# Kernel optimization log

Measured on AMD Instinct MI355X. Metric: run time of the kernel, lower is better.

## Reference

```python
import jax, jax.numpy as jnp
import numpy as np

NUM_EXPERTS = 64
TOP_K = 2
NOISE_STD = 1.0
LOAD_BALANCE_WEIGHT = 0.01
NOISE_KEY = jax.random.fold_in(jax.random.key(0), 12345)


def setup_inputs() -> dict:
    key = jax.random.key(0)
    k1, k2, k3 = jax.random.split(key, 3)
    B, S, D = 4, 4096, 1024
    x = jax.random.normal(k1, (B, S, D), dtype=jnp.float32)
    W_gate = jax.random.normal(k2, (NUM_EXPERTS, D), dtype=jnp.float32) * (1.0 / np.sqrt(D))
    W_noise = jax.random.normal(k3, (NUM_EXPERTS, D), dtype=jnp.float32) * (1.0 / np.sqrt(D))
    return {"x": x, "W_gate": W_gate, "W_noise": W_noise}


def reference(x, W_gate, W_noise):
    # x: [B,S,D], W_gate/W_noise: [E,D] (torch Linear weight layout)
    clean_logits = jnp.einsum("bsd,ed->bse", x, W_gate)           # [B,S,E]
    noise_scale = jax.nn.softplus(jnp.einsum("bsd,ed->bse", x, W_noise))
    noise = jax.random.normal(NOISE_KEY, clean_logits.shape, clean_logits.dtype)
    logits = clean_logits + noise * noise_scale * NOISE_STD

    probs = jax.nn.softmax(logits, axis=-1)                        # [B,S,E]
    routing_weights, expert_indices = jax.lax.top_k(probs, TOP_K)  # [B,S,K]
    routing_weights = routing_weights / jnp.sum(routing_weights, axis=-1, keepdims=True)

    # Load-balance loss on clean logits
    B, S, E = clean_logits.shape
    num_tokens = B * S
    expert_mask = jax.nn.one_hot(expert_indices, E, dtype=jnp.float32).sum(axis=2)  # [B,S,E]
    tokens_per_expert = expert_mask.sum(axis=(0, 1))               # [E]
    fraction_tokens = tokens_per_expert / num_tokens
    router_probs = jax.nn.softmax(clean_logits, axis=-1)
    mean_router_prob = router_probs.mean(axis=(0, 1))              # [E]
    load_balance_loss = LOAD_BALANCE_WEIGHT * E * jnp.sum(fraction_tokens * mean_router_prob)

    noise_scale_mean = noise_scale.mean()
    return (routing_weights, expert_indices, load_balance_loss, router_probs, noise_scale_mean)
```

## Files before the change

kernel.cpp:

```cpp
#include <hip/hip_runtime.h>
#include <stdint.h>

#define TOKENS 16384
#define DDIM   1024
#define NEXP   64
#define NCOL   128
#define TB     32
#define NBLK   (TOKENS / TB)
#define NCH    (DDIM / 32)
#define NTILE  8
#define CPP    8

typedef __attribute__((ext_vector_type(8))) short bf16x8;
typedef __attribute__((ext_vector_type(4))) float f32x4;

__device__ ushort g_wf[3][NTILE][NCH][64][8];
__device__ float g_ps[NEXP];
__device__ float g_cnt[NEXP];
__device__ float g_spa[1];

__device__ inline ushort bf16rne(float f) {
  uint32_t u = __float_as_uint(f);
  return (ushort)((u + 0x7fffu + ((u >> 16) & 1u)) >> 16);
}
__device__ inline float bf16tof(ushort h) {
  return __uint_as_float(((uint32_t)h) << 16);
}
__device__ inline void split3(float v, ushort& h, ushort& m, ushort& l) {
  h = bf16rne(v);
  float r1 = v - bf16tof(h);
  m = bf16rne(r1);
  float r2 = r1 - bf16tof(m);
  l = bf16rne(r2);
}

struct U2 { uint32_t a, b; };

__host__ __device__ constexpr U2 tf2x32(uint32_t k0, uint32_t k1,
                                        uint32_t x0, uint32_t x1) {
  uint32_t ks[3] = {k0, k1, k0 ^ k1 ^ 0x1BD11BDAu};
  const uint32_t rot[2][4] = {{13u, 15u, 26u, 6u}, {17u, 29u, 16u, 24u}};
  x0 += ks[0]; x1 += ks[1];
  for (int d = 0; d < 5; ++d) {
    for (int j = 0; j < 4; ++j) {
      uint32_t r = rot[d & 1][j];
      x0 += x1;
      x1 = (x1 << r) | (x1 >> (32u - r));
      x1 ^= x0;
    }
    x0 += ks[(d + 1) % 3];
    x1 += ks[(d + 2) % 3] + (uint32_t)(d + 1);
  }
  return U2{x0, x1};
}

__device__ inline uint32_t noise_bits(uint32_t i) {
  constexpr U2 NK = tf2x32(0u, 0u, 0u, 12345u);
  U2 o = tf2x32(NK.a, NK.b, 0u, i);
  return o.a ^ o.b;
}

__device__ inline float xla_erfinv(float x) {
  float w = -log1pf(-x * x);
  float p;
  if (w < 5.0f) {
    w = w - 2.5f;
    p = 2.81022636e-08f;
    p = 3.43273939e-07f + p * w;
    p = -3.5233877e-06f + p * w;
    p = -4.39150654e-06f + p * w;
    p = 0.00021858087f + p * w;
    p = -0.00125372503f + p * w;
    p = -0.00417768164f + p * w;
    p = 0.246640727f + p * w;
    p = 1.50140941f + p * w;
  } else {
    w = sqrtf(w) - 3.0f;
    p = -0.000200214257f;
    p = 0.000100950558f + p * w;
    p = 0.00134934322f + p * w;
    p = -0.00367342844f + p * w;
    p = 0.00573950773f + p * w;
    p = -0.0076224613f + p * w;
    p = 0.00943887047f + p * w;
    p = 1.00167406f + p * w;
    p = 2.83297682f + p * w;
  }
  return p * x;
}

__device__ inline float noise_normal(uint32_t i) {
  uint32_t bits = noise_bits(i);
  float f = __uint_as_float((bits >> 9) | 0x3f800000u) - 1.0f;
  float u = f * 2.0f + (-0.99999994f);
  u = fmaxf(u, -0.99999994f);
  return 1.41421356237f * xla_erfinv(u);
}

__device__ inline float softplus_ref(float x) {
  return fmaxf(x, 0.0f) + log1pf(expf(-fabsf(x)));
}

__device__ inline float wave_max64(float v) {
  #pragma unroll
  for (int off = 32; off; off >>= 1) v = fmaxf(v, __shfl_xor(v, off, 64));
  return v;
}
__device__ inline float wave_sum64(float v) {
  #pragma unroll
  for (int off = 32; off; off >>= 1) v += __shfl_xor(v, off, 64);
  return v;
}
__device__ inline void wave_argmax64(float v, int idx, float& mv, int& mi) {
  float bv = v; int bi = idx;
  #pragma unroll
  for (int off = 32; off; off >>= 1) {
    float ov = __shfl_xor(bv, off, 64);
    int   oi = __shfl_xor(bi, off, 64);
    if (ov > bv || (ov == bv && oi < bi)) { bv = ov; bi = oi; }
  }
  mv = bv; mi = bi;
}

__global__ __launch_bounds__(64)
void wsplit_kernel(const float* __restrict__ wg, const float* __restrict__ wn) {
  const int ct   = blockIdx.x >> 5;
  const int kc   = blockIdx.x & 31;
  const int lane = threadIdx.x;
  const int col  = ct * 16 + (lane & 15);
  const int koff = kc * 32 + (lane >> 4) * 8;
  const float* src = (col < NEXP) ? (wg + (size_t)col * DDIM)
                                  : (wn + (size_t)(col - NEXP) * DDIM);
  const float4 v0 = *(const float4*)&src[koff];
  const float4 v1 = *(const float4*)&src[koff + 4];
  const float av[8] = {v0.x, v0.y, v0.z, v0.w, v1.x, v1.y, v1.z, v1.w};
  union BF8 { bf16x8 v; ushort u[8]; };
  BF8 H, M, L;
  #pragma unroll
  for (int j = 0; j < 8; ++j) {
    ushort h, m, l;
    split3(av[j], h, m, l);
    H.u[j] = h; M.u[j] = m; L.u[j] = l;
  }
  *(bf16x8*)&g_wf[0][ct][kc][lane][0] = H.v;
  *(bf16x8*)&g_wf[1][ct][kc][lane][0] = M.v;
  *(bf16x8*)&g_wf[2][ct][kc][lane][0] = L.v;

  if (blockIdx.x == 0) {
    g_ps[lane] = 0.0f; g_cnt[lane] = 0.0f;
    if (lane == 0) g_spa[0] = 0.0f;
  }
}

__global__ __launch_bounds__(1024, 8)
void NoisyTopKRouter_57621281243491_kernel(
    const float* __restrict__ x, float* __restrict__ out) {
  __shared__ ushort ldsA[3][2][CPP][64][8];

  const int tid  = threadIdx.x;
  const int w    = tid >> 6;
  const int lane = tid & 63;
  const int tg   = w & 1;
  const int ct   = w >> 1;
  const int tok0 = blockIdx.x * TB;

  char* LA = (char*)&ldsA[0][0][0][0][0];

  const int srow = tid >> 5;
  const int skq  = tid & 31;
  const int stg  = srow >> 4;
  const int sfr  = srow & 15;
  const int sc   = skq >> 2;
  const int ss   = skq & 3;
  const int so   = (sc * 1024 + ss * 256 + sfr * 16) ^ ((skq & 15) << 4);
  const float* sx = x + (size_t)(tok0 + srow) * DDIM + skq * 8;

  const int fr_row = lane & 15;
  const int fr_s   = lane >> 4;
  const ushort* wf = &g_wf[0][0][0][0][0];
  const int b0 = ct * 16384 + lane * 8;
  #define PS 131072
  const int abase = tg * 8192;

  f32x4 acc = {0.f, 0.f, 0.f, 0.f};

  float4 xa0, xa1, xb0, xb1;

  #define SPLIT_PHASE(X0, X1)                                             \
    {                                                                     \
      union BF8 { bf16x8 v; ushort u[8]; };                               \
      BF8 H, M, L;                                                        \
      const float av_[8] = {X0.x, X0.y, X0.z, X0.w, X1.x, X1.y, X1.z, X1.w}; \
      _Pragma("unroll")                                                   \
      for (int j = 0; j < 8; ++j) {                                       \
        ushort h_, m_, l_;                                                \
        split3(av_[j], h_, m_, l_);                                       \
        H.u[j] = h_; M.u[j] = m_; L.u[j] = l_;                            \
      }                                                                   \
      *(bf16x8*)(LA + stg * 8192 + so)         = H.v;                     \
      *(bf16x8*)(LA + 16384 + stg * 8192 + so) = M.v;                     \
      *(bf16x8*)(LA + 32768 + stg * 8192 + so) = L.v;                     \
    }

  #define MFMA_PHASE(ph)                                                  \
    _Pragma("unroll")                                                     \
    for (int c = 0; c < CPP; ++c) {                                       \
      int ro = c * 1024 + lane * 16;                                      \
      ro ^= ((ro >> 8) & 15) << 4;                                        \
      const bf16x8 Ah = *(const bf16x8*)(LA + abase + ro);                \
      const bf16x8 Am = *(const bf16x8*)(LA + 16384 + abase + ro);        \
      const bf16x8 Al = *(const bf16x8*)(LA + 32768 + abase + ro);        \
      const int co = ((ph) * CPP + c) * 512;                              \
      const bf16x8 Bh = *(const bf16x8*)&wf[b0 + co];                     \
      const bf16x8 Bm = *(const bf16x8*)&wf[b0 + PS + co];                \
      const bf16x8 Bl = *(const bf16x8*)&wf[b0 + 2 * PS + co];            \
      acc = __builtin_amdgcn_mfma_f32_16x16x32_bf16(Ah, Bh, acc, 0, 0, 0); \
      acc = __builtin_amdgcn_mfma_f32_16x16x32_bf16(Ah, Bm, acc, 0, 0, 0); \
      acc = __builtin_amdgcn_mfma_f32_16x16x32_bf16(Am, Bh, acc, 0, 0, 0); \
      acc = __builtin_amdgcn_mfma_f32_16x16x32_bf16(Ah, Bl, acc, 0, 0, 0); \
      acc = __builtin_amdgcn_mfma_f32_16x16x32_bf16(Al, Bh, acc, 0, 0, 0); \
      acc = __builtin_amdgcn_mfma_f32_16x16x32_bf16(Am, Bm, acc, 0, 0, 0); \
    }

  #define DO_PHASE(ph, C0, C1, N0, N1, PRE)                               \
    SPLIT_PHASE(C0, C1);                                                  \
    if (PRE) {                                                            \
      N0 = *(const float4*)&sx[(ph + 1) * 256];                           \
      N1 = *(const float4*)&sx[(ph + 1) * 256 + 4];                       \
    }                                                                     \
    __syncthreads();                                                      \
    MFMA_PHASE(ph);                                                       \
    __syncthreads();

  xa0 = *(const float4*)&sx[0];
  xa1 = *(const float4*)&sx[4];

  DO_PHASE(0, xa0, xa1, xb0, xb1, 1);
  DO_PHASE(1, xb0, xb1, xa0, xa1, 1);
  DO_PHASE(2, xa0, xa1, xb0, xb1, 1);
  DO_PHASE(3, xb0, xb1, xa0, xa1, 0);

  #undef DO_PHASE
  #undef SPLIT_PHASE
  #undef MFMA_PHASE
  #undef PS

  float (*lds_logits)[NCOL + 4] = (float (*)[NCOL + 4])LA;
  float (*lps)[NEXP] = (float (*)[NEXP])(LA + 16896);
  float (*lcb)[NEXP] = (float (*)[NEXP])(LA + 20992);
  float* lspw        = (float*)(LA + 25088);

  #pragma unroll
  for (int r = 0; r < 4; ++r)
    lds_logits[tg * 16 + 4 * fr_s + r][ct * 16 + fr_row] = acc[r];
  __syncthreads();

  float* out_rw  = out;
  float* out_idx = out + 2 * TOKENS;
  float* out_rp  = out + 4 * TOKENS + 1;

  float ps_acc = 0.0f, sp_acc = 0.0f, c_acc = 0.0f;

  for (int it = 0; it < 2; ++it) {
    const int tl = w * 2 + it;
    const int t  = tok0 + tl;
    const float cl = lds_logits[tl][lane];
    const float nl = lds_logits[tl][NEXP + lane];

    const float m  = wave_max64(cl);
    const float v  = expf(cl - m);
    const float Z  = wave_sum64(v);
    const float rp = v / Z;
    out_rp[(size_t)t * NEXP + lane] = rp;
    ps_acc += rp;

    const float ns  = softplus_ref(nl);
    sp_acc += ns;
    const float noi = noise_normal((uint32_t)(t * NEXP + lane));
    const float lgn = __fadd_rn(cl, __fmul_rn(noi, ns));

    const float m2 = wave_max64(lgn);
    const float v2 = expf(lgn - m2);
    const float Z2 = wave_sum64(v2);
    const float p  = v2 / Z2;

    float p1; int i1;
    wave_argmax64(p, lane, p1, i1);
    const float pm = (lane == i1) ? -3.402823466e38f : p;
    float p2; int i2;
    wave_argmax64(pm, lane, p2, i2);

    c_acc += (float)((lane == i1) + (lane == i2));

    if (lane == 0) {
      const float s = p1 + p2;
      out_rw[t * 2 + 0]  = p1 / s;
      out_rw[t * 2 + 1]  = p2 / s;
      out_idx[t * 2 + 0] = (float)i1;
      out_idx[t * 2 + 1] = (float)i2;
    }
  }

  lps[w][lane] = ps_acc;
  lcb[w][lane] = c_acc;
  const float spw = wave_sum64(sp_acc);
  if (lane == 0) lspw[w] = spw;
  __syncthreads();
  if (tid < NEXP) {
    float a = 0.0f, b = 0.0f;
    #pragma unroll
    for (int j = 0; j < 16; ++j) { a += lps[j][tid]; b += lcb[j][tid]; }
    atomicAdd(&g_ps[tid],  a);
    atomicAdd(&g_cnt[tid], b);
  }
  if (tid == 0) {
    float s = 0.0f;
    #pragma unroll
    for (int j = 0; j < 16; ++j) s += lspw[j];
    atomicAdd(&g_spa[0], s);
  }
}

__global__ void finalize_kernel(float* __restrict__ out) {
  const int lane = threadIdx.x;
  float term = (g_cnt[lane] / (float)TOKENS) * (g_ps[lane] / (float)TOKENS);
  #pragma unroll
  for (int off = 32; off; off >>= 1) term += __shfl_xor(term, off, 64);
  if (lane == 0) {
    out[4 * TOKENS] = 0.64f * term;
    out[4 * TOKENS + 1 + TOKENS * NEXP] = g_spa[0] / (float)(TOKENS * NEXP);
  }
}

extern "C" void kernel_launch(void* const* d_in, const int* in_sizes, int n_in,
                              void* d_out, int out_size, void* d_ws, size_t ws_size,
                              hipStream_t stream) {
  const float* x  = (const float*)d_in[0];
  const float* wg = (const float*)d_in[1];
  const float* wn = (const float*)d_in[2];
  float* out = (float*)d_out;

  (void)d_ws; (void)ws_size; (void)in_sizes; (void)n_in; (void)out_size;

  wsplit_kernel<<<NTILE * NCH, 64, 0, stream>>>(wg, wn);
  NoisyTopKRouter_57621281243491_kernel<<<NBLK, 1024, 0, stream>>>(x, out);
  finalize_kernel<<<1, 64, 0, stream>>>(out);
}
```

Before: 144.7 us.

## Fuse weight split and finalize into main kernel using global atomic flags

Removes the separate weight-split and finalize launches. The first 256 blocks of the main kernel now split the weights into bf16 hi/mid/lo parts and signal a global counter, and every block spin-waits on that counter before computing. The last block to finish, found with an atomic ticket, computes the load-balance loss and the noise-scale mean and resets the counters. This saves two kernel launches and their gaps, but every block now depends on the weight-producing blocks being scheduled, since the grid of 512 blocks of 1024 threads must not deadlock. All blocks also pay for the spin-wait and the extra syncs.

```diff
diff --git a/kernel.cpp b/kernel.cpp
--- a/kernel.cpp
+++ b/kernel.cpp
@@ -18,6 +18,8 @@
 __device__ float g_ps[NEXP];
 __device__ float g_cnt[NEXP];
 __device__ float g_spa[1];
+__device__ unsigned g_wdone;
+__device__ unsigned g_done;
 
 __device__ inline ushort bf16rne(float f) {
   uint32_t u = __float_as_uint(f);
@@ -122,49 +124,64 @@
   mv = bv; mi = bi;
 }
 
-__global__ __launch_bounds__(64)
-void wsplit_kernel(const float* __restrict__ wg, const float* __restrict__ wn) {
-  const int ct   = blockIdx.x >> 5;
-  const int kc   = blockIdx.x & 31;
-  const int lane = threadIdx.x;
-  const int col  = ct * 16 + (lane & 15);
-  const int koff = kc * 32 + (lane >> 4) * 8;
-  const float* src = (col < NEXP) ? (wg + (size_t)col * DDIM)
-                                  : (wn + (size_t)(col - NEXP) * DDIM);
-  const float4 v0 = *(const float4*)&src[koff];
-  const float4 v1 = *(const float4*)&src[koff + 4];
-  const float av[8] = {v0.x, v0.y, v0.z, v0.w, v1.x, v1.y, v1.z, v1.w};
-  union BF8 { bf16x8 v; ushort u[8]; };
-  BF8 H, M, L;
-  #pragma unroll
-  for (int j = 0; j < 8; ++j) {
-    ushort h, m, l;
-    split3(av[j], h, m, l);
-    H.u[j] = h; M.u[j] = m; L.u[j] = l;
-  }
-  *(bf16x8*)&g_wf[0][ct][kc][lane][0] = H.v;
-  *(bf16x8*)&g_wf[1][ct][kc][lane][0] = M.v;
-  *(bf16x8*)&g_wf[2][ct][kc][lane][0] = L.v;
-
-  if (blockIdx.x == 0) {
-    g_ps[lane] = 0.0f; g_cnt[lane] = 0.0f;
-    if (lane == 0) g_spa[0] = 0.0f;
-  }
-}
-
 __global__ __launch_bounds__(1024, 8)
 void NoisyTopKRouter_57621281243491_kernel(
-    const float* __restrict__ x, float* __restrict__ out) {
+    const float* __restrict__ x, const float* __restrict__ wg,
+    const float* __restrict__ wn, float* __restrict__ out) {
   __shared__ ushort ldsA[3][2][CPP][64][8];
 
   const int tid  = threadIdx.x;
+  const int bid  = blockIdx.x;
   const int w    = tid >> 6;
   const int lane = tid & 63;
   const int tg   = w & 1;
   const int ct   = w >> 1;
-  const int tok0 = blockIdx.x * TB;
+  const int tok0 = bid * TB;
 
   char* LA = (char*)&ldsA[0][0][0][0][0];
+
+  if (bid < NTILE * NCH) {
+    if (tid < 64) {
+      const int act  = bid >> 5;
+      const int akc  = bid & 31;
+      const int col  = act * 16 + (tid & 15);
+      const int koff = akc * 32 + (tid >> 4) * 8;
+      const float* src = (col < NEXP) ? (wg + (size_t)col * DDIM)
+                                      : (wn + (size_t)(col - NEXP) * DDIM);
+      const float4 v0 = *(const float4*)&src[koff];
+      const float4 v1 = *(const float4*)&src[koff + 4];
+      const float av[8] = {v0.x, v0.y, v0.z, v0.w, v1.x, v1.y, v1.z, v1.w};
+      union BF8 { bf16x8 v; ushort u[8]; };
+      BF8 H, M, L;
+      #pragma unroll
+      for (int j = 0; j < 8; ++j) {
+        ushort h, m, l;
+        split3(av[j], h, m, l);
+        H.u[j] = h; M.u[j] = m; L.u[j] = l;
+      }
+      *(bf16x8*)&g_wf[0][act][akc][tid][0] = H.v;
+      *(bf16x8*)&g_wf[1][act][akc][tid][0] = M.v;
+      *(bf16x8*)&g_wf[2][act][akc][tid][0] = L.v;
+    }
+    if (bid == 0) {
+      if (tid >= 64 && tid < 128) { g_ps[tid - 64] = 0.0f; g_cnt[tid - 64] = 0.0f; }
+      if (tid == 128) g_spa[0] = 0.0f;
+    }
+    __syncthreads();
+    if (tid == 0) {
+      __threadfence();
+      __hip_atomic_fetch_add(&g_wdone, 1u, __ATOMIC_RELEASE,
+                             __HIP_MEMORY_SCOPE_AGENT);
+    }
+  }
+
+  if (tid == 0) {
+    while (__hip_atomic_load(&g_wdone, __ATOMIC_ACQUIRE,
+                             __HIP_MEMORY_SCOPE_AGENT) < (unsigned)(NTILE * NCH))
+      __builtin_amdgcn_s_sleep(2);
+    __threadfence();
+  }
+  __syncthreads();
 
   const int srow = tid >> 5;
   const int skq  = tid & 31;
@@ -319,16 +336,34 @@
     for (int j = 0; j < 16; ++j) s += lspw[j];
     atomicAdd(&g_spa[0], s);
   }
-}
-
-__global__ void finalize_kernel(float* __restrict__ out) {
-  const int lane = threadIdx.x;
-  float term = (g_cnt[lane] / (float)TOKENS) * (g_ps[lane] / (float)TOKENS);
-  #pragma unroll
-  for (int off = 32; off; off >>= 1) term += __shfl_xor(term, off, 64);
-  if (lane == 0) {
-    out[4 * TOKENS] = 0.64f * term;
-    out[4 * TOKENS + 1 + TOKENS * NEXP] = g_spa[0] / (float)(TOKENS * NEXP);
+
+  __syncthreads();
+  __shared__ int s_last;
+  if (tid == 0) {
+    __threadfence();
+    const unsigned prev = __hip_atomic_fetch_add(&g_done, 1u, __ATOMIC_ACQ_REL,
+                                                 __HIP_MEMORY_SCOPE_AGENT);
+    s_last = (prev == (unsigned)(NBLK - 1)) ? 1 : 0;
+  }
+  __syncthreads();
+  if (s_last) {
+    if (tid < NEXP) {
+      const float cnt = __hip_atomic_load(&g_cnt[tid], __ATOMIC_RELAXED,
+                                          __HIP_MEMORY_SCOPE_AGENT);
+      const float ps  = __hip_atomic_load(&g_ps[tid],  __ATOMIC_RELAXED,
+                                          __HIP_MEMORY_SCOPE_AGENT);
+      float term = (cnt / (float)TOKENS) * (ps / (float)TOKENS);
+      #pragma unroll
+      for (int off = 32; off; off >>= 1) term += __shfl_xor(term, off, 64);
+      if (tid == 0) {
+        out[4 * TOKENS] = 0.64f * term;
+        const float spa = __hip_atomic_load(&g_spa[0], __ATOMIC_RELAXED,
+                                            __HIP_MEMORY_SCOPE_AGENT);
+        out[4 * TOKENS + 1 + TOKENS * NEXP] = spa / (float)(TOKENS * NEXP);
+        __hip_atomic_store(&g_done, 0u, __ATOMIC_RELAXED, __HIP_MEMORY_SCOPE_AGENT);
+        __hip_atomic_store(&g_wdone, 0u, __ATOMIC_RELAXED, __HIP_MEMORY_SCOPE_AGENT);
+      }
+    }
   }
 }
 
@@ -342,7 +377,5 @@
 
   (void)d_ws; (void)ws_size; (void)in_sizes; (void)n_in; (void)out_size;
 
-  wsplit_kernel<<<NTILE * NCH, 64, 0, stream>>>(wg, wn);
-  NoisyTopKRouter_57621281243491_kernel<<<NBLK, 1024, 0, stream>>>(x, out);
-  finalize_kernel<<<1, 64, 0, stream>>>(out);
-}
+  NoisyTopKRouter_57621281243491_kernel<<<NBLK, 1024, 0, stream>>>(x, wg, wn, out);
+}
```

Measured after the change: 189.0 us. +30.7%, slower.
